# Optimization experiments

Hardware: AMD Instinct MI355X
Metric: run time of the kernel (lower is better)

## Reference

```python
import jax, jax.numpy as jnp
import numpy as np
import math

D_MODEL = 128
N_HEADS = 4
DIM_FF = 256
B, L = 4, 2048
EPS = 1e-5
NEG = -1e9


def _layernorm(x, g, b):
    mu = jnp.mean(x, axis=-1, keepdims=True)
    var = jnp.mean((x - mu) ** 2, axis=-1, keepdims=True)
    return (x - mu) * jax.lax.rsqrt(var + EPS) * g + b


def setup_inputs() -> dict:
    key = jax.random.key(0)
    ks = jax.random.split(key, 16)
    s = 1.0 / math.sqrt(D_MODEL)
    return {
        "h": jax.random.normal(ks[0], (B, L, D_MODEL), jnp.float32),
        "attn_bias": jax.random.normal(ks[1], (B, N_HEADS, L, L), jnp.float32),
        "node_mask": jax.random.randint(ks[2], (B, L), 0, 2).astype(jnp.float32),
        "sparse_mask": jax.random.randint(ks[3], (B, L, L), 0, 2).astype(bool),
        "w_qkv": jax.random.normal(ks[4], (3 * D_MODEL, D_MODEL), jnp.float32) * s,
        "b_qkv": jnp.zeros((3 * D_MODEL,), jnp.float32),
        "w_out": jax.random.normal(ks[5], (D_MODEL, D_MODEL), jnp.float32) * s,
        "b_out": jnp.zeros((D_MODEL,), jnp.float32),
        "w_ff1": jax.random.normal(ks[6], (DIM_FF, D_MODEL), jnp.float32) * s,
        "b_ff1": jnp.zeros((DIM_FF,), jnp.float32),
        "w_ff2": jax.random.normal(ks[7], (D_MODEL, DIM_FF), jnp.float32) * (1.0 / math.sqrt(DIM_FF)),
        "b_ff2": jnp.zeros((D_MODEL,), jnp.float32),
        "ln1_g": jnp.ones((D_MODEL,), jnp.float32),
        "ln1_b": jnp.zeros((D_MODEL,), jnp.float32),
        "ln2_g": jnp.ones((D_MODEL,), jnp.float32),
        "ln2_b": jnp.zeros((D_MODEL,), jnp.float32),
    }


def reference(h, attn_bias, node_mask, sparse_mask, w_qkv, b_qkv, w_out, b_out,
              w_ff1, b_ff1, w_ff2, b_ff2, ln1_g, ln1_b, ln2_g, ln2_b):
    bsz, lsz, dsz = h.shape
    dk = dsz // N_HEADS
    qkv = h @ w_qkv.T + b_qkv  # [B,L,3D]
    q, k, v = jnp.split(qkv, 3, axis=-1)
    # [B,L,D] -> [B,H,L,dk]
    q = q.reshape(bsz, lsz, N_HEADS, dk).transpose(0, 2, 1, 3)
    k = k.reshape(bsz, lsz, N_HEADS, dk).transpose(0, 2, 1, 3)
    v = v.reshape(bsz, lsz, N_HEADS, dk).transpose(0, 2, 1, 3)
    scores = jnp.einsum("bhqd,bhkd->bhqk", q, k) / math.sqrt(dk)
    scores = scores + attn_bias
    scores = jnp.where(sparse_mask[:, None, :, :], scores, NEG)
    key_mask = node_mask[:, None, None, :] > 0
    scores = jnp.where(key_mask, scores, NEG)
    attn = jax.nn.softmax(scores, axis=-1)
    attn = attn * (node_mask[:, None, :, None] > 0).astype(attn.dtype)
    out = jnp.einsum("bhqk,bhkd->bhqd", attn, v)
    out = out.transpose(0, 2, 1, 3).reshape(bsz, lsz, dsz)
    out = out @ w_out.T + b_out
    h1 = _layernorm(h + out, ln1_g, ln1_b)
    ff = jax.nn.relu(h1 @ w_ff1.T + b_ff1) @ w_ff2.T + b_ff2
    h2 = _layernorm(h1 + ff, ln2_g, ln2_b)
    return h2 * node_mask[:, :, None]
```

## Files before the change

kernel.cpp:

```cpp
#include <hip/hip_runtime.h>
#include <math.h>

#define NEG_INF (-1e9f)
#define EPS 1e-5f

typedef __attribute__((ext_vector_type(8))) short short8;
typedef __attribute__((ext_vector_type(4))) float floatx4;

__device__ __forceinline__ unsigned short f2bf(float x) {
    union { float f; unsigned u; } v; v.f = x;
    unsigned r = v.u + 0x7fffu + ((v.u >> 16) & 1u);
    return (unsigned short)(r >> 16);
}

__device__ __forceinline__ void gl2lds16(const void* g, void* l) {
    __builtin_amdgcn_global_load_lds(
        (const __attribute__((address_space(1))) unsigned int*)g,
        (__attribute__((address_space(3))) unsigned int*)l, 16, 0, 0);
}

__global__ void transpose_prep_kernel(const float* __restrict__ w_qkv, const float* __restrict__ w_out,
                                      const float* __restrict__ w_ff1, const float* __restrict__ w_ff2,
                                      float* __restrict__ wqkvT, float* __restrict__ woutT,
                                      float* __restrict__ wff1T, float* __restrict__ wff2T,
                                      const unsigned int* __restrict__ sm, int* __restrict__ flag,
                                      const float* __restrict__ nm, unsigned int* __restrict__ nmb) {
    if (blockIdx.x < 512) {
        int idx = blockIdx.x * 256 + threadIdx.x;
        if (idx < 49152) {
            int r = idx / 128, c = idx % 128;
            wqkvT[c * 384 + r] = w_qkv[idx];
        } else if (idx < 65536) {
            int i = idx - 49152; int r = i / 128, c = i % 128;
            woutT[c * 128 + r] = w_out[i];
        } else if (idx < 98304) {
            int i = idx - 65536; int r = i / 128, c = i % 128;
            wff1T[c * 256 + r] = w_ff1[i];
        } else {
            int i = idx - 98304; int r = i / 256, c = i % 256;
            wff2T[c * 128 + r] = w_ff2[i];
        }
    } else if (blockIdx.x == 512) {
        __shared__ int bad;
        if (threadIdx.x == 0) bad = 0;
        __syncthreads();
        for (int i = threadIdx.x; i < 4096; i += 256) {
            if (sm[i] > 1u) bad = 1;
        }
        __syncthreads();
        if (threadIdx.x == 0) *flag = bad;
    } else {
        const int t = threadIdx.x;
        const int b = t >> 6, w32 = t & 63;
        unsigned u = 0;
#pragma unroll
        for (int j = 0; j < 32; ++j)
            u |= (nm[b * 2048 + w32 * 32 + j] > 0.f ? 1u : 0u) << j;
        nmb[t] = u;
    }
}

__global__ void mask_prep_kernel(const unsigned char* __restrict__ smraw,
                                 const int* __restrict__ flag,
                                 const unsigned int* __restrict__ nmb,
                                 unsigned int* __restrict__ cbits) {
    const int idx = blockIdx.x * 256 + threadIdx.x;
    const int b = idx >> 17;
    const int q = (idx >> 6) & 2047;
    const int w32 = idx & 63;
    unsigned u = 0;
    if (*flag) {
        const uint4* p = reinterpret_cast<const uint4*>(
            smraw + (size_t)(b * 2048 + q) * 2048 + w32 * 32);
        uint4 a = p[0], c = p[1];
        unsigned wd0 = a.x, wd1 = a.y, wd2 = a.z, wd3 = a.w;
        unsigned wd4 = c.x, wd5 = c.y, wd6 = c.z, wd7 = c.w;
#define BYTES4(v, sh) \
        u |= ((v) & 0xffu ? 1u : 0u) << (sh); \
        u |= ((v) & 0xff00u ? 1u : 0u) << ((sh) + 1); \
        u |= ((v) & 0xff0000u ? 1u : 0u) << ((sh) + 2); \
        u |= ((v) & 0xff000000u ? 1u : 0u) << ((sh) + 3);
        BYTES4(wd0, 0) BYTES4(wd1, 4) BYTES4(wd2, 8) BYTES4(wd3, 12)
        BYTES4(wd4, 16) BYTES4(wd5, 20) BYTES4(wd6, 24) BYTES4(wd7, 28)
#undef BYTES4
    } else {
        const uint4* p = reinterpret_cast<const uint4*>(
            reinterpret_cast<const unsigned int*>(smraw) + (size_t)(b * 2048 + q) * 2048 + w32 * 32);
#pragma unroll
        for (int wi = 0; wi < 8; ++wi) {
            uint4 a = p[wi];
            u |= (a.x ? 1u : 0u) << (wi * 4);
            u |= (a.y ? 1u : 0u) << (wi * 4 + 1);
            u |= (a.z ? 1u : 0u) << (wi * 4 + 2);
            u |= (a.w ? 1u : 0u) << (wi * 4 + 3);
        }
    }
    cbits[idx] = u & nmb[b * 64 + w32];
}

__global__ void qkv_kernel(const float* __restrict__ h, const float* __restrict__ wT,
                           const float* __restrict__ bqkv,
                           unsigned short* __restrict__ qb, unsigned short* __restrict__ kbm,
                           unsigned short* __restrict__ vtb) {
    __shared__ __align__(16) float hs[16 * 128];
    const int tid = threadIdx.x;
    const int row0 = blockIdx.x * 16;
    for (int i = tid; i < 2048; i += 384) hs[i] = h[row0 * 128 + i];
    __syncthreads();

    const int c = tid;
    float acc[16];
#pragma unroll
    for (int r = 0; r < 16; ++r) acc[r] = 0.f;

    for (int d0 = 0; d0 < 128; d0 += 4) {
        float w0 = wT[(d0 + 0) * 384 + c];
        float w1 = wT[(d0 + 1) * 384 + c];
        float w2 = wT[(d0 + 2) * 384 + c];
        float w3 = wT[(d0 + 3) * 384 + c];
#pragma unroll
        for (int r = 0; r < 16; ++r) {
            float4 h4 = *reinterpret_cast<const float4*>(&hs[r * 128 + d0]);
            acc[r] = fmaf(w0, h4.x, acc[r]);
            acc[r] = fmaf(w1, h4.y, acc[r]);
            acc[r] = fmaf(w2, h4.z, acc[r]);
            acc[r] = fmaf(w3, h4.w, acc[r]);
        }
    }
    const int part = c >> 7;
    const int cc = c & 127;
    const int head = cc >> 5;
    const int dd = cc & 31;
    const float bias = bqkv[c];
    const float scale = (part == 0) ? 0.17677669529663687f : 1.0f;
#pragma unroll
    for (int r = 0; r < 16; ++r) {
        int grow = row0 + r;
        int b = grow >> 11, l = grow & 2047;
        int bh = b * 4 + head;
        unsigned short val = f2bf((acc[r] + bias) * scale);
        if (part == 0)      qb[((size_t)bh * 2048 + l) * 32 + dd] = val;
        else if (part == 1) kbm[((size_t)bh * 2048 + l) * 32 + dd] = val;
        else                vtb[((size_t)bh * 32 + dd) * 2048 + l] = val;
    }
}

__global__ __launch_bounds__(256, 2) void attn_kernel(
        const unsigned short* __restrict__ qb, const unsigned short* __restrict__ kbm,
        const unsigned short* __restrict__ vtb, const float* __restrict__ bias,
        const unsigned int* __restrict__ cbits, const float* __restrict__ nmask,
        float* __restrict__ aout) {
    __shared__ __align__(16) unsigned short k_lds[2][64 * 32];
    __shared__ __align__(16) unsigned short v_lds[2][32 * 64];
    __shared__ __align__(16) float bias_lds[4][32 * 64];
    __shared__ __align__(16) unsigned short p_lds[4][16 * 40];
    __shared__ float merge_lds[2][64][10];

    const int tid = threadIdx.x;
    const int w = tid >> 6, L = tid & 63;
    const int qsub = w & 1, khalf = w >> 1;
    const int lb = (blockIdx.x & 7) * 128 + (blockIdx.x >> 3);
    const int bh = lb >> 6, qt = lb & 63;
    const int b = bh >> 2, hh = bh & 3;
    const int q0b = qt * 32;
    const int q = L & 15, g = L >> 4;

    const unsigned short* kb_g = kbm + (size_t)bh * 2048 * 32;
    const unsigned short* vb_g = vtb + (size_t)bh * 32 * 2048;
    const float* bias_q0 = bias + ((size_t)bh * 2048 + q0b) * 2048;
    const short8 qf = *reinterpret_cast<const short8*>(
        qb + ((size_t)bh * 2048 + q0b + qsub * 16 + q) * 32 + g * 8);
    const unsigned int* crow = cbits + (size_t)(b * 2048 + q0b + qsub * 16 + q) * 64;

    const int krow = tid >> 2, kc = tid & 3;
    const int kf_st = (krow & 3) ^ ((krow >> 2) & 3);
    const int vrow = tid >> 3, vc = tid & 7;

    auto stage_kv = [&](int buf, int kt) {
        const int k0 = kt * 64;
        gl2lds16(kb_g + (size_t)(k0 + krow) * 32 + ((kc ^ kf_st) << 3),
                 (char*)(&k_lds[buf][0]) + w * 1024);
        gl2lds16(vb_g + (size_t)vrow * 2048 + k0 + ((vc ^ (vrow & 7)) << 3),
                 (char*)(&v_lds[buf][0]) + w * 1024);
    };
    auto stage_bias = [&](int buf, int kt) {
        const int k0 = kt * 64;
#pragma unroll
        for (int i = 0; i < 2; ++i) {
            int row = i * 16 + (tid >> 4);
            int csrc = (tid & 15) ^ (row & 7);
            gl2lds16(bias_q0 + (size_t)row * 2048 + k0 + (csrc << 2),
                     (char*)(&bias_lds[buf][0]) + i * 4096 + w * 1024);
        }
    };

    stage_kv(0, 0);
    stage_bias(0, 0);
    stage_kv(1, 1);
    stage_bias(1, 1);
    stage_bias(2, 2);
    asm volatile("s_waitcnt vmcnt(6)" ::: "memory");
    __builtin_amdgcn_s_barrier();

    float mrun = -3.0e38f, lrun = 0.f;
    floatx4 o0 = {0.f, 0.f, 0.f, 0.f}, o1 = {0.f, 0.f, 0.f, 0.f};
    const floatx4 zacc = {0.f, 0.f, 0.f, 0.f};
    unsigned short* pl = &p_lds[w][q * 40];

    const int r0k = khalf * 32 + q;
    const int fk = (q & 3) ^ ((q >> 2) & 3);
    const int koff0 = r0k * 64 + ((g ^ fk) << 4);
    const int koff1 = (r0k + 16) * 64 + ((g ^ fk) << 4);
    const int vch = khalf * 4 + g;
    const int voff0 = q * 128 + ((vch ^ (q & 7)) << 4);
    const int voff1 = (16 + q) * 128 + ((vch ^ (q & 7)) << 4);
    const int R = qsub * 16 + q;
    const int j0 = khalf * 8 + g;
    const int boff0 = R * 256 + (((j0    ) ^ (R & 7)) << 4);
    const int boff1 = R * 256 + (((j0 + 4) ^ (R & 7)) << 4);

    for (int t = 0; t < 32; ++t) {
        const int cur = t & 1;
        const int bcur = t & 3;

        const char* kl = (const char*)(&k_lds[cur][0]);
        short8 kf0 = *reinterpret_cast<const short8*>(kl + koff0);
        short8 kf1 = *reinterpret_cast<const short8*>(kl + koff1);
        const char* vl = (const char*)(&v_lds[cur][0]);
        short8 vf0 = *reinterpret_cast<const short8*>(vl + voff0);
        short8 vf1 = *reinterpret_cast<const short8*>(vl + voff1);
        const char* bl = (const char*)(&bias_lds[bcur][0]);
        float4 bq0 = *reinterpret_cast<const float4*>(bl + boff0);
        float4 bq1 = *reinterpret_cast<const float4*>(bl + boff1);
        const unsigned cw = crow[2 * t + khalf];

        floatx4 rr0 = __builtin_amdgcn_mfma_f32_16x16x32_bf16(kf0, qf, zacc, 0, 0, 0);
        floatx4 rr1 = __builtin_amdgcn_mfma_f32_16x16x32_bf16(kf1, qf, zacc, 0, 0, 0);
        float s[8];
        s[0] = rr0[0]; s[1] = rr0[1]; s[2] = rr0[2]; s[3] = rr0[3];
        s[4] = rr1[0]; s[5] = rr1[1]; s[6] = rr1[2]; s[7] = rr1[3];
        float bvv[8];
        bvv[0] = bq0.x; bvv[1] = bq0.y; bvv[2] = bq0.z; bvv[3] = bq0.w;
        bvv[4] = bq1.x; bvv[5] = bq1.y; bvv[6] = bq1.z; bvv[7] = bq1.w;
#pragma unroll
        for (int i = 0; i < 8; ++i) {
            const int mm = i >> 2, reg = i & 3;
            const int sh = mm * 16 + 4 * g + reg;
            const bool keep = (cw >> sh) & 1;
            s[i] = keep ? (s[i] + bvv[i]) : NEG_INF;
        }
        float tm = s[0];
#pragma unroll
        for (int i = 1; i < 8; ++i) tm = fmaxf(tm, s[i]);
        tm = fmaxf(tm, __shfl_xor(tm, 16));
        tm = fmaxf(tm, __shfl_xor(tm, 32));
        const float mn = fmaxf(mrun, tm);
        const float f = __expf(mrun - mn);
        mrun = mn;
        float p[8], ts = 0.f;
#pragma unroll
        for (int i = 0; i < 8; ++i) { p[i] = __expf(s[i] - mn); ts += p[i]; }
        ts += __shfl_xor(ts, 16);
        ts += __shfl_xor(ts, 32);
        lrun = lrun * f + ts;
        o0 *= f; o1 *= f;
        {
            unsigned u0 = (unsigned)f2bf(p[0]) | ((unsigned)f2bf(p[1]) << 16);
            unsigned u1 = (unsigned)f2bf(p[2]) | ((unsigned)f2bf(p[3]) << 16);
            unsigned u2 = (unsigned)f2bf(p[4]) | ((unsigned)f2bf(p[5]) << 16);
            unsigned u3 = (unsigned)f2bf(p[6]) | ((unsigned)f2bf(p[7]) << 16);
            *reinterpret_cast<unsigned int*>(pl + 4 * g) = u0;
            *reinterpret_cast<unsigned int*>(pl + 4 * g + 2) = u1;
            *reinterpret_cast<unsigned int*>(pl + 16 + 4 * g) = u2;
            *reinterpret_cast<unsigned int*>(pl + 16 + 4 * g + 2) = u3;
        }
        short8 pb = *reinterpret_cast<const short8*>(pl + 8 * g);
        o0 = __builtin_amdgcn_mfma_f32_16x16x32_bf16(vf0, pb, o0, 0, 0, 0);
        o1 = __builtin_amdgcn_mfma_f32_16x16x32_bf16(vf1, pb, o1, 0, 0, 0);

        if (t < 31) {
            __builtin_amdgcn_s_barrier();
            const int kt2 = (t + 2 > 31) ? 31 : t + 2;
            const int bt3 = (t + 3 > 31) ? 31 : t + 3;
            stage_kv(cur, kt2);
            stage_bias((t + 3) & 3, bt3);
            asm volatile("s_waitcnt vmcnt(6)" ::: "memory");
            __builtin_amdgcn_s_barrier();
        }
    }

    if (khalf == 1) {
        float* dst = merge_lds[qsub][L];
        dst[0] = mrun; dst[1] = lrun;
        dst[2] = o0[0]; dst[3] = o0[1]; dst[4] = o0[2]; dst[5] = o0[3];
        dst[6] = o1[0]; dst[7] = o1[1]; dst[8] = o1[2]; dst[9] = o1[3];
    }
    __syncthreads();
    if (khalf == 0) {
        const float* src = merge_lds[qsub][L];
        const float m2 = src[0], l2 = src[1];
        const float mm = fmaxf(mrun, m2);
        const float f1 = __expf(mrun - mm), f2 = __expf(m2 - mm);
        const float l = lrun * f1 + l2 * f2;
        const int qrow = q0b + qsub * 16 + q;
        const float nmq = nmask[b * 2048 + qrow];
        const float inv = (nmq > 0.f) ? (1.f / l) : 0.f;
        const float a1 = f1 * inv, a2 = f2 * inv;
        float* op = aout + ((size_t)b * 2048 + qrow) * 128 + hh * 32 + g * 4;
        *reinterpret_cast<float4*>(op) = make_float4(
            o0[0] * a1 + src[2] * a2, o0[1] * a1 + src[3] * a2,
            o0[2] * a1 + src[4] * a2, o0[3] * a1 + src[5] * a2);
        *reinterpret_cast<float4*>(op + 16) = make_float4(
            o1[0] * a1 + src[6] * a2, o1[1] * a1 + src[7] * a2,
            o1[2] * a1 + src[8] * a2, o1[3] * a1 + src[9] * a2);
    }
}

__device__ __forceinline__ void ln_stats(const float* buf, float* mu_s, float* rs_s, int tid) {
    int row = tid >> 4, sl = tid & 15;
    float4 x0 = *reinterpret_cast<const float4*>(&buf[row * 128 + sl * 8]);
    float4 x1 = *reinterpret_cast<const float4*>(&buf[row * 128 + sl * 8 + 4]);
    float sum = x0.x + x0.y + x0.z + x0.w + x1.x + x1.y + x1.z + x1.w;
    float sq = x0.x * x0.x + x0.y * x0.y + x0.z * x0.z + x0.w * x0.w +
               x1.x * x1.x + x1.y * x1.y + x1.z * x1.z + x1.w * x1.w;
#pragma unroll
    for (int off = 8; off > 0; off >>= 1) {
        sum += __shfl_xor(sum, off);
        sq += __shfl_xor(sq, off);
    }
    if (sl == 0) {
        float mu = sum * (1.f / 128.f);
        float var = sq * (1.f / 128.f) - mu * mu;
        mu_s[row] = mu;
        rs_s[row] = rsqrtf(var + EPS);
    }
}

__global__ void epilogue_kernel(const float* __restrict__ aout, const float* __restrict__ h,
                                const float* __restrict__ woutT, const float* __restrict__ bout,
                                const float* __restrict__ wff1T, const float* __restrict__ bff1,
                                const float* __restrict__ wff2T, const float* __restrict__ bff2,
                                const float* __restrict__ g1, const float* __restrict__ b1,
                                const float* __restrict__ g2, const float* __restrict__ b2,
                                const float* __restrict__ nmask, float* __restrict__ out) {
    __shared__ __align__(16) float A[16 * 128];
    __shared__ __align__(16) float Hb[16 * 128];
    __shared__ __align__(16) float F[16 * 256];
    __shared__ float mu_s[16], rs_s[16];

    const int tid = threadIdx.x;
    const int row0 = blockIdx.x * 16;
    for (int i = tid; i < 2048; i += 256) {
        A[i] = aout[row0 * 128 + i];
        Hb[i] = h[row0 * 128 + i];
    }
    __syncthreads();

    const int g = tid >> 7, c = tid & 127;

    float acc[8];
#pragma unroll
    for (int r = 0; r < 8; ++r) acc[r] = 0.f;
    for (int d0 = 0; d0 < 128; d0 += 4) {
        float w0 = woutT[(d0 + 0) * 128 + c];
        float w1 = woutT[(d0 + 1) * 128 + c];
        float w2 = woutT[(d0 + 2) * 128 + c];
        float w3 = woutT[(d0 + 3) * 128 + c];
#pragma unroll
        for (int r = 0; r < 8; ++r) {
            float4 a4 = *reinterpret_cast<const float4*>(&A[(g * 8 + r) * 128 + d0]);
            acc[r] = fmaf(w0, a4.x, acc[r]);
            acc[r] = fmaf(w1, a4.y, acc[r]);
            acc[r] = fmaf(w2, a4.z, acc[r]);
            acc[r] = fmaf(w3, a4.w, acc[r]);
        }
    }
    float bo = bout[c];
#pragma unroll
    for (int r = 0; r < 8; ++r) {
        int row = g * 8 + r;
        Hb[row * 128 + c] += acc[r] + bo;
    }
    __syncthreads();

    ln_stats(Hb, mu_s, rs_s, tid);
    __syncthreads();
    float g1c = g1[c], b1c = b1[c];
#pragma unroll
    for (int r = 0; r < 8; ++r) {
        int row = g * 8 + r;
        float v = (Hb[row * 128 + c] - mu_s[row]) * rs_s[row] * g1c + b1c;
        Hb[row * 128 + c] = v;
    }
    __syncthreads();

    {
        const int j = tid;
        float a2[16];
#pragma unroll
        for (int r = 0; r < 16; ++r) a2[r] = 0.f;
        for (int d0 = 0; d0 < 128; d0 += 4) {
            float w0 = wff1T[(d0 + 0) * 256 + j];
            float w1 = wff1T[(d0 + 1) * 256 + j];
            float w2 = wff1T[(d0 + 2) * 256 + j];
            float w3 = wff1T[(d0 + 3) * 256 + j];
#pragma unroll
            for (int r = 0; r < 16; ++r) {
                float4 h4 = *reinterpret_cast<const float4*>(&Hb[r * 128 + d0]);
                a2[r] = fmaf(w0, h4.x, a2[r]);
                a2[r] = fmaf(w1, h4.y, a2[r]);
                a2[r] = fmaf(w2, h4.z, a2[r]);
                a2[r] = fmaf(w3, h4.w, a2[r]);
            }
        }
        float bj = bff1[j];
#pragma unroll
        for (int r = 0; r < 16; ++r) F[r * 256 + j] = fmaxf(a2[r] + bj, 0.f);
    }
    __syncthreads();

    float a3[8];
#pragma unroll
    for (int r = 0; r < 8; ++r) a3[r] = 0.f;
    for (int d0 = 0; d0 < 256; d0 += 4) {
        float w0 = wff2T[(d0 + 0) * 128 + c];
        float w1 = wff2T[(d0 + 1) * 128 + c];
        float w2 = wff2T[(d0 + 2) * 128 + c];
        float w3 = wff2T[(d0 + 3) * 128 + c];
#pragma unroll
        for (int r = 0; r < 8; ++r) {
            float4 f4 = *reinterpret_cast<const float4*>(&F[(g * 8 + r) * 256 + d0]);
            a3[r] = fmaf(w0, f4.x, a3[r]);
            a3[r] = fmaf(w1, f4.y, a3[r]);
            a3[r] = fmaf(w2, f4.z, a3[r]);
            a3[r] = fmaf(w3, f4.w, a3[r]);
        }
    }
    float bo2 = bff2[c];
#pragma unroll
    for (int r = 0; r < 8; ++r) {
        int row = g * 8 + r;
        A[row * 128 + c] = a3[r] + bo2 + Hb[row * 128 + c];
    }
    __syncthreads();

    ln_stats(A, mu_s, rs_s, tid);
    __syncthreads();
    float g2c = g2[c], b2c = b2[c];
#pragma unroll
    for (int r = 0; r < 8; ++r) {
        int row = g * 8 + r;
        float nm = nmask[row0 + row];
        float v = (A[row * 128 + c] - mu_s[row]) * rs_s[row] * g2c + b2c;
        out[(row0 + row) * 128 + c] = v * nm;
    }
}

extern "C" void kernel_launch(void* const* d_in, const int* in_sizes, int n_in,
                              void* d_out, int out_size, void* d_ws, size_t ws_size,
                              hipStream_t stream) {
    const float* h = (const float*)d_in[0];
    const float* bias = (const float*)d_in[1];
    const float* nmask = (const float*)d_in[2];
    const void* smask = d_in[3];
    const float* w_qkv = (const float*)d_in[4];
    const float* b_qkv = (const float*)d_in[5];
    const float* w_out = (const float*)d_in[6];
    const float* b_out = (const float*)d_in[7];
    const float* w_ff1 = (const float*)d_in[8];
    const float* b_ff1 = (const float*)d_in[9];
    const float* w_ff2 = (const float*)d_in[10];
    const float* b_ff2 = (const float*)d_in[11];
    const float* g1 = (const float*)d_in[12];
    const float* b1 = (const float*)d_in[13];
    const float* g2 = (const float*)d_in[14];
    const float* b2 = (const float*)d_in[15];
    float* out = (float*)d_out;

    char* wsb = (char*)d_ws;
    float* aoutw = (float*)wsb;
    unsigned short* qb  = (unsigned short*)(wsb + (4 << 20));
    unsigned short* kbm = (unsigned short*)(wsb + (6 << 20));
    unsigned short* vtb = (unsigned short*)(wsb + (8 << 20));
    unsigned int* cbits = (unsigned int*)(wsb + (10 << 20));
    unsigned int* nmb   = (unsigned int*)(wsb + (12 << 20));
    float* wqkvT = (float*)(wsb + (12 << 20) + 4096);
    float* woutT = wqkvT + 384 * 128;
    float* wff1T = woutT + 128 * 128;
    float* wff2T = wff1T + 256 * 128;
    int* smflag = (int*)(wff2T + 128 * 256);

    transpose_prep_kernel<<<514, 256, 0, stream>>>(w_qkv, w_out, w_ff1, w_ff2,
                                                   wqkvT, woutT, wff1T, wff2T,
                                                   (const unsigned int*)smask, smflag,
                                                   nmask, nmb);
    mask_prep_kernel<<<2048, 256, 0, stream>>>((const unsigned char*)smask, smflag, nmb, cbits);
    qkv_kernel<<<512, 384, 0, stream>>>(h, wqkvT, b_qkv, qb, kbm, vtb);
    attn_kernel<<<1024, 256, 0, stream>>>(qb, kbm, vtb, bias, cbits, nmask, aoutw);
    epilogue_kernel<<<512, 256, 0, stream>>>(aoutw, h, woutT, b_out, wff1T, b_ff1,
                                             wff2T, b_ff2, g1, b1, g2, b2, nmask, out);
}
```

Measured before the change: 181.2 us.

## Shrink attention LDS footprint to fit four blocks per CU

```diff
diff --git a/kernel.cpp b/kernel.cpp
--- a/kernel.cpp
+++ b/kernel.cpp
@@ -145,16 +145,15 @@
     }
 }
 
-__global__ __launch_bounds__(256, 2) void attn_kernel(
+__global__ __launch_bounds__(256, 4) void attn_kernel(
         const unsigned short* __restrict__ qb, const unsigned short* __restrict__ kbm,
         const unsigned short* __restrict__ vtb, const float* __restrict__ bias,
         const unsigned int* __restrict__ cbits, const float* __restrict__ nmask,
         float* __restrict__ aout) {
     __shared__ __align__(16) unsigned short k_lds[2][64 * 32];
     __shared__ __align__(16) unsigned short v_lds[2][32 * 64];
-    __shared__ __align__(16) float bias_lds[4][32 * 64];
+    __shared__ __align__(16) float bias_lds[2][32 * 64];
     __shared__ __align__(16) unsigned short p_lds[4][16 * 40];
-    __shared__ float merge_lds[2][64][10];
 
     const int tid = threadIdx.x;
     const int w = tid >> 6, L = tid & 63;
@@ -175,31 +174,25 @@
     const int krow = tid >> 2, kc = tid & 3;
     const int kf_st = (krow & 3) ^ ((krow >> 2) & 3);
     const int vrow = tid >> 3, vc = tid & 7;
-
-    auto stage_kv = [&](int buf, int kt) {
+    const int brow0 = tid >> 4, bc = tid & 15;
+
+    auto stage = [&](int buf, int kt) {
         const int k0 = kt * 64;
         gl2lds16(kb_g + (size_t)(k0 + krow) * 32 + ((kc ^ kf_st) << 3),
                  (char*)(&k_lds[buf][0]) + w * 1024);
         gl2lds16(vb_g + (size_t)vrow * 2048 + k0 + ((vc ^ (vrow & 7)) << 3),
                  (char*)(&v_lds[buf][0]) + w * 1024);
+#pragma unroll
+        for (int i = 0; i < 2; ++i) {
+            const int row = i * 16 + brow0;
+            gl2lds16(bias_q0 + (size_t)row * 2048 + k0 + ((bc ^ (row & 7)) << 2),
+                     (char*)(&bias_lds[buf][0]) + i * 4096 + w * 1024);
+        }
     };
-    auto stage_bias = [&](int buf, int kt) {
-        const int k0 = kt * 64;
-#pragma unroll
-        for (int i = 0; i < 2; ++i) {
-            int row = i * 16 + (tid >> 4);
-            int csrc = (tid & 15) ^ (row & 7);
-            gl2lds16(bias_q0 + (size_t)row * 2048 + k0 + (csrc << 2),
-                     (char*)(&bias_lds[buf][0]) + i * 4096 + w * 1024);
-        }
-    };
-
-    stage_kv(0, 0);
-    stage_bias(0, 0);
-    stage_kv(1, 1);
-    stage_bias(1, 1);
-    stage_bias(2, 2);
-    asm volatile("s_waitcnt vmcnt(6)" ::: "memory");
+
+    stage(0, 0);
+    stage(1, 1);
+    asm volatile("s_waitcnt vmcnt(4)" ::: "memory");
     __builtin_amdgcn_s_barrier();
 
     float mrun = -3.0e38f, lrun = 0.f;
@@ -221,7 +214,6 @@
 
     for (int t = 0; t < 32; ++t) {
         const int cur = t & 1;
-        const int bcur = t & 3;
 
         const char* kl = (const char*)(&k_lds[cur][0]);
         short8 kf0 = *reinterpret_cast<const short8*>(kl + koff0);
@@ -229,7 +221,7 @@
         const char* vl = (const char*)(&v_lds[cur][0]);
         short8 vf0 = *reinterpret_cast<const short8*>(vl + voff0);
         short8 vf1 = *reinterpret_cast<const short8*>(vl + voff1);
-        const char* bl = (const char*)(&bias_lds[bcur][0]);
+        const char* bl = (const char*)(&bias_lds[cur][0]);
         float4 bq0 = *reinterpret_cast<const float4*>(bl + boff0);
         float4 bq1 = *reinterpret_cast<const float4*>(bl + boff1);
         const unsigned cw = crow[2 * t + khalf];
@@ -280,24 +272,27 @@
 
         if (t < 31) {
             __builtin_amdgcn_s_barrier();
-            const int kt2 = (t + 2 > 31) ? 31 : t + 2;
-            const int bt3 = (t + 3 > 31) ? 31 : t + 3;
-            stage_kv(cur, kt2);
-            stage_bias((t + 3) & 3, bt3);
-            asm volatile("s_waitcnt vmcnt(6)" ::: "memory");
+            if (t + 2 < 32) {
+                stage(cur, t + 2);
+                asm volatile("s_waitcnt vmcnt(4)" ::: "memory");
+            } else {
+                asm volatile("s_waitcnt vmcnt(0)" ::: "memory");
+            }
             __builtin_amdgcn_s_barrier();
         }
     }
 
+    __syncthreads();
+    float* mb = reinterpret_cast<float*>(&p_lds[0][0]);
     if (khalf == 1) {
-        float* dst = merge_lds[qsub][L];
+        float* dst = mb + (qsub * 64 + L) * 10;
         dst[0] = mrun; dst[1] = lrun;
         dst[2] = o0[0]; dst[3] = o0[1]; dst[4] = o0[2]; dst[5] = o0[3];
         dst[6] = o1[0]; dst[7] = o1[1]; dst[8] = o1[2]; dst[9] = o1[3];
     }
     __syncthreads();
     if (khalf == 0) {
-        const float* src = merge_lds[qsub][L];
+        const float* src = mb + (qsub * 64 + L) * 10;
         const float m2 = src[0], l2 = src[1];
         const float mm = fmaxf(mrun, m2);
         const float f1 = __expf(mrun - mm), f2 = __expf(m2 - mm);
```

Result: faster. 165.7 us (-8.5%).
